# Performance work log

Measured on AMD Instinct MI355X. Metric: run time of the kernel, lower is better.

Reference implementation:

```python
import jax, jax.numpy as jnp
import numpy as np


def setup_inputs() -> dict:
    key = jax.random.key(0)
    k1, k2, k3 = jax.random.split(key, 3)
    B, N, C_IN, C_OUT = 8, 2048, 128, 64
    x = jax.random.normal(k1, (B, N, C_IN), dtype=jnp.float32)
    # Linear(c_in, c_out): weight [c_out, c_in], bias [c_out]
    W_adj = jax.random.normal(k2, (C_OUT, C_IN), dtype=jnp.float32) * (1.0 / np.sqrt(C_IN))
    b_adj = jax.random.normal(k3, (C_OUT,), dtype=jnp.float32) * 0.01
    return {"x": x, "W_adj": W_adj, "b_adj": b_adj}


def reference(x, W_adj, b_adj):
    # e_x = adj_projection(x): [B, N, C_out]
    e_x = jnp.einsum("bnc,oc->bno", x, W_adj) + b_adj
    # The original loop/concat builds all (i, j) pairs and takes per-pair
    # inner products; this is exactly the Gram matrix e_x @ e_x^T.
    lp = jax.nn.relu(jnp.tanh(jnp.einsum("bic,bjc->bij", e_x, e_x)))  # [B, N, N]
    num_neighbours = x.shape[1]
    node_feats = jnp.einsum("bij,bjc->bic", lp, e_x) / num_neighbours
    return node_feats, lp
```

## Files before the change

### kernel.cpp

```cpp
#include <hip/hip_runtime.h>
#include <hip/hip_bf16.h>


#define B_    8
#define N_    2048
#define D_    64
#define CIN_  128

typedef __bf16 bf16x8 __attribute__((ext_vector_type(8)));
typedef float f32x4  __attribute__((ext_vector_type(4)));
typedef float f32x16 __attribute__((ext_vector_type(16)));

union FragU { uint4 u; bf16x8 f; };

static __device__ __forceinline__ bf16x8 ld_frag(const __hip_bfloat16* p) {
    FragU fu; fu.u = *reinterpret_cast<const uint4*>(p); return fu.f;
}

static __device__ __forceinline__ void split8(const float* p, bf16x8& hi, bf16x8& lo) {
    const float4 a = *reinterpret_cast<const float4*>(p);
    const float4 b = *reinterpret_cast<const float4*>(p + 4);
    const float v[8] = {a.x, a.y, a.z, a.w, b.x, b.y, b.z, b.w};
#pragma unroll
    for (int i = 0; i < 8; i++) {
        const __bf16 h = (__bf16)v[i];
        hi[i] = h;
        lo[i] = (__bf16)(v[i] - (float)h);
    }
}

__global__ __launch_bounds__(256) void wsplit_kernel(
    const float* __restrict__ W,
    __hip_bfloat16* __restrict__ whi,
    __hip_bfloat16* __restrict__ wlo)
{
    const int tid = threadIdx.x;
#pragma unroll
    for (int k = 0; k < 8; k++) {
        const float4 v = reinterpret_cast<const float4*>(W)[tid * 8 + k];
        const int idx = tid * 32 + k * 4;
        const float vv[4] = {v.x, v.y, v.z, v.w};
#pragma unroll
        for (int j = 0; j < 4; j++) {
            const __hip_bfloat16 h = __float2bfloat16(vv[j]);
            whi[idx + j] = h;
            wlo[idx + j] = __float2bfloat16(vv[j] - __bfloat162float(h));
        }
    }
}

__global__ __launch_bounds__(256) void ex_kernel(
    const float* __restrict__ x,
    const __hip_bfloat16* __restrict__ whi,
    const __hip_bfloat16* __restrict__ wlo,
    const float* __restrict__ bias,
    __hip_bfloat16* __restrict__ e_hi,
    __hip_bfloat16* __restrict__ e_lo,
    __hip_bfloat16* __restrict__ e_hiT)
{
    __shared__ __align__(16) __hip_bfloat16 sEh[64 * 72];
    __shared__ __align__(16) __hip_bfloat16 sEl[64 * 72];
    __shared__ __align__(16) __hip_bfloat16 sEt[64 * 72];

    const int tid  = threadIdx.x;
    const int w    = tid >> 6;
    const int lane = tid & 63;
    const int quad = lane >> 4;
    const int l16  = lane & 15;
    const int gr0  = blockIdx.x * 64;
    const int m0   = gr0 + w * 16;

    const float* xrow = x + (size_t)(m0 + l16) * CIN_;
    bf16x8 ah[4], al[4];
#pragma unroll
    for (int ks = 0; ks < 4; ks++)
        split8(xrow + ks * 32 + quad * 8, ah[ks], al[ks]);

    f32x4 acc[4];
#pragma unroll
    for (int nt = 0; nt < 4; nt++) acc[nt] = f32x4{0.f, 0.f, 0.f, 0.f};

#pragma unroll
    for (int ks = 0; ks < 4; ks++) {
#pragma unroll
        for (int nt = 0; nt < 4; nt++) {
            const bf16x8 wh = ld_frag(whi + (nt * 16 + l16) * CIN_ + ks * 32 + quad * 8);
            const bf16x8 wl = ld_frag(wlo + (nt * 16 + l16) * CIN_ + ks * 32 + quad * 8);
            acc[nt] = __builtin_amdgcn_mfma_f32_16x16x32_bf16(ah[ks], wh, acc[nt], 0, 0, 0);
            acc[nt] = __builtin_amdgcn_mfma_f32_16x16x32_bf16(ah[ks], wl, acc[nt], 0, 0, 0);
            acc[nt] = __builtin_amdgcn_mfma_f32_16x16x32_bf16(al[ks], wh, acc[nt], 0, 0, 0);
        }
    }

#pragma unroll
    for (int nt = 0; nt < 4; nt++) {
        const int chan = nt * 16 + l16;
        const float bv = bias[chan];
#pragma unroll
        for (int i = 0; i < 4; i++) {
            const int rl = w * 16 + quad * 4 + i;
            const float e = acc[nt][i] + bv;
            const __hip_bfloat16 hi = __float2bfloat16(e);
            const __hip_bfloat16 lo = __float2bfloat16(e - __bfloat162float(hi));
            sEh[rl * 72 + chan] = hi;
            sEl[rl * 72 + chan] = lo;
            sEt[chan * 72 + rl] = hi;
        }
    }
    __syncthreads();

    const int bt = gr0 >> 11, ir0 = gr0 & (N_ - 1);
#pragma unroll
    for (int p = 0; p < 2; p++) {
        const int q = tid + p * 256;
        const int r = q >> 3, c = (q & 7) * 8;
        *(uint4*)(e_hi + (size_t)(gr0 + r) * D_ + c)  = *(const uint4*)(sEh + r * 72 + c);
        *(uint4*)(e_lo + (size_t)(gr0 + r) * D_ + c)  = *(const uint4*)(sEl + r * 72 + c);
        *(uint4*)(e_hiT + ((size_t)bt * D_ + r) * N_ + ir0 + c) = *(const uint4*)(sEt + r * 72 + c);
    }
}

#define LT 136

__global__ __launch_bounds__(512) void fused_kernel(
    const __hip_bfloat16* __restrict__ e_hi,
    const __hip_bfloat16* __restrict__ e_lo,
    const __hip_bfloat16* __restrict__ e_hiT,
    float* __restrict__ out)
{
    __shared__ __align__(16) __hip_bfloat16 sLp[64 * LT];
    __shared__ __align__(16) float sO[8 * 32 * 64];

    const int b   = blockIdx.x;
    const int i0  = blockIdx.y * 64;
    const int tid = threadIdx.x;
    const int w = tid >> 6, lane = tid & 63;
    const int l32 = lane & 31, half = lane >> 5;
    const int quad = lane >> 4, l16 = lane & 15;
    const int g2 = w >> 2, h2 = w & 3;

    const __hip_bfloat16* eih = e_hi + (size_t)(b * N_ + i0 + g2 * 32 + l32) * D_;
    const __hip_bfloat16* eil = e_lo + (size_t)(b * N_ + i0 + g2 * 32 + l32) * D_;
    bf16x8 ahi[4], alo[4];
#pragma unroll
    for (int ks = 0; ks < 4; ks++) {
        ahi[ks] = ld_frag(eih + ks * 16 + half * 8);
        alo[ks] = ld_frag(eil + ks * 16 + half * 8);
    }

    f32x4 o[2][4];
#pragma unroll
    for (int mt = 0; mt < 2; mt++)
#pragma unroll
        for (int nt = 0; nt < 4; nt++) o[mt][nt] = f32x4{0.f, 0.f, 0.f, 0.f};

    float* lp_out = out + (size_t)B_ * N_ * D_;

    for (int jt = 0; jt < 16; jt++) {
        const int j0 = jt * 128;

        const __hip_bfloat16* ejh = e_hi + (size_t)(b * N_ + j0 + h2 * 32 + l32) * D_;
        const __hip_bfloat16* ejl = e_lo + (size_t)(b * N_ + j0 + h2 * 32 + l32) * D_;
        f32x16 s = {};
#pragma unroll
        for (int ks = 0; ks < 4; ks++) {
            const bf16x8 bh = ld_frag(ejh + ks * 16 + half * 8);
            const bf16x8 bl = ld_frag(ejl + ks * 16 + half * 8);
            s = __builtin_amdgcn_mfma_f32_32x32x16_bf16(ahi[ks], bh, s, 0, 0, 0);
            s = __builtin_amdgcn_mfma_f32_32x32x16_bf16(ahi[ks], bl, s, 0, 0, 0);
            s = __builtin_amdgcn_mfma_f32_32x32x16_bf16(alo[ks], bh, s, 0, 0, 0);
        }

#pragma unroll
        for (int r = 0; r < 16; r++) {
            const int rl = (r & 3) + 8 * (r >> 2) + 4 * half;
            const float tc = fmaxf(s[r], 0.0f);
            const float z = __builtin_amdgcn_exp2f(tc * -2.8853900817779268f);
            const float v = (1.0f - z) * __builtin_amdgcn_rcpf(1.0f + z);
            lp_out[(size_t)(b * N_ + i0 + g2 * 32 + rl) * N_ + j0 + h2 * 32 + l32] = v;
            sLp[(g2 * 32 + rl) * LT + h2 * 32 + l32] = __float2bfloat16(v);
        }

        __builtin_amdgcn_s_waitcnt(0xc07f);

#pragma unroll
        for (int mt = 0; mt < 2; mt++) {
            const bf16x8 a = ld_frag(sLp + (g2 * 32 + mt * 16 + l16) * LT + h2 * 32 + quad * 8);
#pragma unroll
            for (int nt = 0; nt < 4; nt++) {
                const bf16x8 bfr = ld_frag(e_hiT + ((size_t)b * D_ + nt * 16 + l16) * N_
                                           + j0 + h2 * 32 + quad * 8);
                o[mt][nt] = __builtin_amdgcn_mfma_f32_16x16x32_bf16(a, bfr, o[mt][nt], 0, 0, 0);
            }
        }
    }

    __syncthreads();
#pragma unroll
    for (int mt = 0; mt < 2; mt++)
#pragma unroll
        for (int nt = 0; nt < 4; nt++)
#pragma unroll
            for (int i = 0; i < 4; i++)
                sO[w * 2048 + (mt * 16 + quad * 4 + i) * 64 + nt * 16 + l16] = o[mt][nt][i];
    __syncthreads();
#pragma unroll
    for (int p = 0; p < 8; p++) {
        const int q = tid + p * 512;
        const int row = q >> 6, chan = q & 63;
        const int gg = row >> 5, rl = row & 31;
        float v = 0.f;
#pragma unroll
        for (int hh = 0; hh < 4; hh++)
            v += sO[(gg * 4 + hh) * 2048 + rl * 64 + chan];
        out[(size_t)(b * N_ + i0 + row) * D_ + chan] = v * (1.0f / 2048.0f);
    }
}

extern "C" void kernel_launch(void* const* d_in, const int* in_sizes, int n_in,
                              void* d_out, int out_size, void* d_ws, size_t ws_size,
                              hipStream_t stream) {
    const float* x    = (const float*)d_in[0];
    const float* W    = (const float*)d_in[1];
    const float* bias = (const float*)d_in[2];
    float* out = (float*)d_out;

    __hip_bfloat16* e_hi  = (__hip_bfloat16*)d_ws;
    __hip_bfloat16* e_lo  = e_hi + (size_t)B_ * N_ * D_;
    __hip_bfloat16* e_hiT = e_lo + (size_t)B_ * N_ * D_;
    __hip_bfloat16* whi   = e_hiT + (size_t)B_ * N_ * D_;
    __hip_bfloat16* wlo   = whi + D_ * CIN_;

    wsplit_kernel<<<dim3(1), dim3(256), 0, stream>>>(W, whi, wlo);
    ex_kernel<<<dim3(256), dim3(256), 0, stream>>>(x, whi, wlo, bias, e_hi, e_lo, e_hiT);
    fused_kernel<<<dim3(8, 32), dim3(512), 0, stream>>>(e_hi, e_lo, e_hiT, out);
}
```

Before: 184.3 us.

## Fuse weight split into projection, nontemporal lp stores, hoist B-fragment loads

Removes the separate weight-splitting kernel, so the projection kernel now reads fp32 weights and splits them into bf16 hi/lo pairs in registers. The large lp output is written with nontemporal stores to reduce cache pollution from the 134MB stream. The transposed e fragments are loaded once per tile before the MFMA loop rather than inside it. Together these save a kernel launch and some redundant loads, at the cost of extra conversion arithmetic in every projection block.

```diff
diff --git a/kernel.cpp b/kernel.cpp
--- a/kernel.cpp
+++ b/kernel.cpp
@@ -29,30 +29,9 @@
     }
 }
 
-__global__ __launch_bounds__(256) void wsplit_kernel(
-    const float* __restrict__ W,
-    __hip_bfloat16* __restrict__ whi,
-    __hip_bfloat16* __restrict__ wlo)
-{
-    const int tid = threadIdx.x;
-#pragma unroll
-    for (int k = 0; k < 8; k++) {
-        const float4 v = reinterpret_cast<const float4*>(W)[tid * 8 + k];
-        const int idx = tid * 32 + k * 4;
-        const float vv[4] = {v.x, v.y, v.z, v.w};
-#pragma unroll
-        for (int j = 0; j < 4; j++) {
-            const __hip_bfloat16 h = __float2bfloat16(vv[j]);
-            whi[idx + j] = h;
-            wlo[idx + j] = __float2bfloat16(vv[j] - __bfloat162float(h));
-        }
-    }
-}
-
 __global__ __launch_bounds__(256) void ex_kernel(
     const float* __restrict__ x,
-    const __hip_bfloat16* __restrict__ whi,
-    const __hip_bfloat16* __restrict__ wlo,
+    const float* __restrict__ W,
     const float* __restrict__ bias,
     __hip_bfloat16* __restrict__ e_hi,
     __hip_bfloat16* __restrict__ e_lo,
@@ -84,8 +63,8 @@
     for (int ks = 0; ks < 4; ks++) {
 #pragma unroll
         for (int nt = 0; nt < 4; nt++) {
-            const bf16x8 wh = ld_frag(whi + (nt * 16 + l16) * CIN_ + ks * 32 + quad * 8);
-            const bf16x8 wl = ld_frag(wlo + (nt * 16 + l16) * CIN_ + ks * 32 + quad * 8);
+            bf16x8 wh, wl;
+            split8(W + (size_t)(nt * 16 + l16) * CIN_ + ks * 32 + quad * 8, wh, wl);
             acc[nt] = __builtin_amdgcn_mfma_f32_16x16x32_bf16(ah[ks], wh, acc[nt], 0, 0, 0);
             acc[nt] = __builtin_amdgcn_mfma_f32_16x16x32_bf16(ah[ks], wl, acc[nt], 0, 0, 0);
             acc[nt] = __builtin_amdgcn_mfma_f32_16x16x32_bf16(al[ks], wh, acc[nt], 0, 0, 0);
@@ -177,21 +156,24 @@
             const float tc = fmaxf(s[r], 0.0f);
             const float z = __builtin_amdgcn_exp2f(tc * -2.8853900817779268f);
             const float v = (1.0f - z) * __builtin_amdgcn_rcpf(1.0f + z);
-            lp_out[(size_t)(b * N_ + i0 + g2 * 32 + rl) * N_ + j0 + h2 * 32 + l32] = v;
+            __builtin_nontemporal_store(
+                v, lp_out + (size_t)(b * N_ + i0 + g2 * 32 + rl) * N_ + j0 + h2 * 32 + l32);
             sLp[(g2 * 32 + rl) * LT + h2 * 32 + l32] = __float2bfloat16(v);
         }
 
         __builtin_amdgcn_s_waitcnt(0xc07f);
 
+        bf16x8 bfr[4];
+#pragma unroll
+        for (int nt = 0; nt < 4; nt++)
+            bfr[nt] = ld_frag(e_hiT + ((size_t)b * D_ + nt * 16 + l16) * N_
+                              + j0 + h2 * 32 + quad * 8);
 #pragma unroll
         for (int mt = 0; mt < 2; mt++) {
             const bf16x8 a = ld_frag(sLp + (g2 * 32 + mt * 16 + l16) * LT + h2 * 32 + quad * 8);
 #pragma unroll
-            for (int nt = 0; nt < 4; nt++) {
-                const bf16x8 bfr = ld_frag(e_hiT + ((size_t)b * D_ + nt * 16 + l16) * N_
-                                           + j0 + h2 * 32 + quad * 8);
-                o[mt][nt] = __builtin_amdgcn_mfma_f32_16x16x32_bf16(a, bfr, o[mt][nt], 0, 0, 0);
-            }
+            for (int nt = 0; nt < 4; nt++)
+                o[mt][nt] = __builtin_amdgcn_mfma_f32_16x16x32_bf16(a, bfr[nt], o[mt][nt], 0, 0, 0);
         }
     }
 
@@ -228,10 +210,7 @@
     __hip_bfloat16* e_hi  = (__hip_bfloat16*)d_ws;
     __hip_bfloat16* e_lo  = e_hi + (size_t)B_ * N_ * D_;
     __hip_bfloat16* e_hiT = e_lo + (size_t)B_ * N_ * D_;
-    __hip_bfloat16* whi   = e_hiT + (size_t)B_ * N_ * D_;
-    __hip_bfloat16* wlo   = whi + D_ * CIN_;
-
-    wsplit_kernel<<<dim3(1), dim3(256), 0, stream>>>(W, whi, wlo);
-    ex_kernel<<<dim3(256), dim3(256), 0, stream>>>(x, whi, wlo, bias, e_hi, e_lo, e_hiT);
+
+    ex_kernel<<<dim3(256), dim3(256), 0, stream>>>(x, W, bias, e_hi, e_lo, e_hiT);
     fused_kernel<<<dim3(8, 32), dim3(512), 0, stream>>>(e_hi, e_lo, e_hiT, out);
 }
```

Measured after the change: 186.5 us. No clear change (+1.2%).
